# Performance work log

Hardware: AMD Instinct MI355X
Metric: run time of the kernel (lower is better)

## Reference

```python
import jax, jax.numpy as jnp
import numpy as np

N = 262144          # pixels (512x512 image)
F = 2               # in_features (x, y)
K = 13              # num_frequencies
H = 256             # dim_hidden
OUT = 3             # out_features (RGB)
TILES = [1, 4, 16, 64, 256]   # prod(tile_dims[i]) per layer
PE_DIM = F + 2 * F * K        # 54


def setup_inputs() -> dict:
    key = jax.random.key(0)
    ks = jax.random.split(key, 2 * len(TILES) + 3)
    inp = {"coords": jax.random.uniform(ks[0], (N, F), dtype=jnp.float32)}
    d_in = PE_DIM
    for i, t in enumerate(TILES):
        # kaiming-uniform-like scale; biases init to zero as in the module
        bound = float(np.sqrt(6.0 / d_in))
        inp[f"w{i}"] = jax.random.uniform(ks[1 + i], (t, d_in, H), dtype=jnp.float32,
                                           minval=-bound, maxval=bound)
        inp[f"b{i}"] = jnp.zeros((H,), dtype=jnp.float32)
        d_in = H
    bound = float(np.sqrt(6.0 / H))
    inp["w_last"] = jax.random.uniform(ks[-1], (OUT, H), dtype=jnp.float32,
                                        minval=-bound, maxval=bound)
    inp["b_last"] = jnp.zeros((OUT,), dtype=jnp.float32)
    return inp


def _pos_enc(coords):
    # NeRF positional encoding, concat order: coords, then for each freq i,
    # for each feature j: sin(2^i * pi * c_j), cos(2^i * pi * c_j)
    freqs = (2.0 ** jnp.arange(K, dtype=jnp.float32)) * np.pi      # [K]
    ang = coords[:, None, :] * freqs[None, :, None]                # [N, K, F]
    enc = jnp.stack([jnp.sin(ang), jnp.cos(ang)], axis=-1)         # [N, K, F, 2]
    enc = enc.reshape(coords.shape[0], 2 * K * F)
    return jnp.concatenate([coords, enc], axis=-1)                 # [N, PE_DIM]


def reference(coords, w0, b0, w1, b1, w2, b2, w3, b3, w4, b4, w_last, b_last):
    x = _pos_enc(coords)                                           # [N, 54]
    for w, b in ((w0, b0), (w1, b1), (w2, b2), (w3, b3), (w4, b4)):
        t = w.shape[0]
        x = x.reshape(t, -1, x.shape[-1])                          # [T, N/T, d_in]
        x = jnp.einsum('tnd,tdo->tno', x, w) + b                   # per-tile GEMM
        x = jnp.where(x > 0, x, 0.2 * x)                           # LeakyReLU(0.2)
    x = x.reshape(-1, H)                                           # [N, H]
    return x @ w_last.T + b_last                                   # [N, OUT]
```

## Files before the change

kernel.cpp:

```cpp
#include <hip/hip_runtime.h>
#include <stdint.h>

typedef uint32_t u32;
typedef short s16x8 __attribute__((ext_vector_type(8)));
typedef float f32x16 __attribute__((ext_vector_type(16)));
typedef u32 u32x2 __attribute__((ext_vector_type(2)));
typedef u32 u32x4 __attribute__((ext_vector_type(4)));

#define NPIX   262144
#define HD     256

#define FTHR      256
#define PXB       128
#define NBLK      (NPIX / PXB)
#define ACT_LDS   65536

#define B0_OFF  0u
#define B1_OFF  32768u
#define B2_OFF  557056u
#define B3_OFF  2654208u
#define B4_OFF  11042816u
#define BH_OFF  44597248u
#define BLOB_TOTAL 44613632u
#define F_W1 2048u
#define F_W2 34816u
#define F_W3 165888u
#define F_W4 690176u
#define F_WH 2787328u
#define F_END 2788352u

#define ACT_BYTES  131072
#define WBUF_BYTES 16384
#define FB_LDS     (ACT_BYTES + 2 * WBUF_BYTES)

__device__ __forceinline__ u32 bfpair(float a, float b) {
    u32 ua = __builtin_bit_cast(u32, a);
    u32 ub = __builtin_bit_cast(u32, b);
    ua = (ua + 0x7FFFu + ((ua >> 16) & 1u)) >> 16;
    ub = (ub + 0x7FFFu + ((ub >> 16) & 1u)) >> 16;
    return ua | (ub << 16);
}
__device__ __forceinline__ u32 act_off(int row, int colByte) {
    return (u32)((row << 9) + (colByte ^ ((row & 31) << 4)));
}
__device__ __forceinline__ u32 w_off32(int col, int kByte) {
    return (u32)((col << 6) + (kByte ^ (((col >> 1) & 3) << 4)));
}

extern "C" __global__ __launch_bounds__(256)
void loe_prepass(const float* __restrict__ w0, const float* __restrict__ w1,
                 const float* __restrict__ w2, const float* __restrict__ w3,
                 const float* __restrict__ w4, const float* __restrict__ wl,
                 char* __restrict__ ws)
{
    const u32 f = blockIdx.x * 256 + threadIdx.x;
    if (f >= F_END) return;
    float v[8];
    char* dst;
    if (f < F_W1) {
        const u32 kk = f >> 9, fb = (f >> 6) & 7, lane = f & 63;
        const u32 l31 = lane & 31, lhi = lane >> 5;
        const u32 k0 = kk * 16 + lhi * 8, col = fb * 32 + l31;
        #pragma unroll
        for (int j = 0; j < 8; ++j)
            v[j] = (k0 + j < 54) ? w0[(k0 + j) * HD + col] : 0.0f;
        dst = ws + B0_OFF + (size_t)f * 16;
    } else if (f < F_WH) {
        const float* W; size_t boff; u32 fl;
        if (f < F_W2)      { W = w1; boff = B1_OFF; fl = f - F_W1; }
        else if (f < F_W3) { W = w2; boff = B2_OFF; fl = f - F_W2; }
        else if (f < F_W4) { W = w3; boff = B3_OFF; fl = f - F_W3; }
        else               { W = w4; boff = B4_OFF; fl = f - F_W4; }
        const u32 t = fl >> 13, c = fl & 8191;
        const u32 kk = c >> 9, fb = (c >> 6) & 7, lane = c & 63;
        const u32 l31 = lane & 31, lhi = lane >> 5;
        const u32 k0 = kk * 16 + lhi * 8, col = fb * 32 + l31;
        const float* src = W + (size_t)t * 65536 + (size_t)k0 * HD + col;
        #pragma unroll
        for (int j = 0; j < 8; ++j) v[j] = src[(size_t)j * HD];
        dst = ws + boff + (size_t)fl * 16;
    } else {
        const u32 fl = f - F_WH;
        const u32 kk = fl >> 6, lane = fl & 63;
        const u32 l31 = lane & 31, lhi = lane >> 5;
        const u32 k0 = kk * 16 + lhi * 8;
        #pragma unroll
        for (int j = 0; j < 8; ++j)
            v[j] = (l31 < 3) ? wl[l31 * HD + k0 + j] : 0.0f;
        dst = ws + BH_OFF + (size_t)fl * 16;
    }
    u32x4 pk;
    pk.x = bfpair(v[0], v[1]); pk.y = bfpair(v[2], v[3]);
    pk.z = bfpair(v[4], v[5]); pk.w = bfpair(v[6], v[7]);
    *reinterpret_cast<u32x4*>(dst) = pk;
}

extern "C" __global__ __launch_bounds__(FTHR, 2)
void loe_fused_pre(const float* __restrict__ coords,
                   const float* __restrict__ b0, const float* __restrict__ b1,
                   const float* __restrict__ b2, const float* __restrict__ b3,
                   const float* __restrict__ b4, const float* __restrict__ bl,
                   const char* __restrict__ blob,
                   float* __restrict__ out)
{
    extern __shared__ char lds[];

    const int tid  = threadIdx.x;
    const int lane = tid & 63;
    const int wv   = tid >> 6;
    const int l31  = lane & 31;
    const int lhi  = lane >> 5;

    const int bid  = (int)blockIdx.x;
    const int pb   = ((bid & 7) << 8) | (bid >> 3);
    const int pix0 = pb << 7;

    {
        const int p = tid >> 1;
        const int h = tid & 1;
        const float2 c2 = reinterpret_cast<const float2*>(coords)[pix0 + p];
        const float cf[2] = {c2.x, c2.y};
        #pragma unroll
        for (int u = 0; u < 32; u += 2) {
            float v[2];
            #pragma unroll
            for (int q = 0; q < 2; ++q) {
                const int c = h * 32 + u + q;
                float val;
                if (c < 2) val = cf[c];
                else if (c - 2 >= 52) val = 0.0f;
                else {
                    const int e = c - 2;
                    const float a = cf[(e >> 1) & 1] * (float)(1 << (e >> 2));
                    val = (e & 1) ? cospif(a) : sinpif(a);
                }
                v[q] = val;
            }
            *reinterpret_cast<u32*>(lds + act_off(p, (h * 32 + u) * 2)) = bfpair(v[0], v[1]);
        }
    }

    f32x16 acc[4][2];
    const u32 swz = (u32)(l31 << 4);
    u32 abase[4];
    #pragma unroll
    for (int pt = 0; pt < 4; ++pt) abase[pt] = (u32)((pt * 32 + l31) << 9);

    auto init_acc = [&](const float* Bias) {
        #pragma unroll
        for (int ct = 0; ct < 2; ++ct)
            #pragma unroll
            for (int q = 0; q < 4; ++q) {
                const float4 bv = *reinterpret_cast<const float4*>(Bias + wv * 64 + ct * 32 + q * 8 + lhi * 4);
                #pragma unroll
                for (int pt = 0; pt < 4; ++pt) {
                    acc[pt][ct][q * 4 + 0] = bv.x; acc[pt][ct][q * 4 + 1] = bv.y;
                    acc[pt][ct][q * 4 + 2] = bv.z; acc[pt][ct][q * 4 + 3] = bv.w;
                }
            }
    };

    auto epilogue = [&]() {
        #pragma unroll
        for (int ct = 0; ct < 2; ++ct)
            #pragma unroll
            for (int q = 0; q < 4; ++q) {
                const int oc0 = wv * 64 + ct * 32 + q * 8 + lhi * 4;
                #pragma unroll
                for (int pt = 0; pt < 4; ++pt) {
                    float x[4];
                    #pragma unroll
                    for (int j = 0; j < 4; ++j) {
                        const float v = acc[pt][ct][q * 4 + j];
                        x[j] = fmaxf(v, 0.2f * v);
                    }
                    u32x2 wo;
                    wo.x = bfpair(x[0], x[1]);
                    wo.y = bfpair(x[2], x[3]);
                    *reinterpret_cast<u32x2*>(lds + act_off(pt * 32 + l31, oc0 * 2)) = wo;
                }
            }
    };

    auto run_layer = [&](int KK, const char* wbase, const float* Bias) {
        init_acc(Bias);
        __syncthreads();
        const char* f0 = wbase + (size_t)(wv * 2) * 1024 + (size_t)lane * 16;
        u32x4 wA = *reinterpret_cast<const u32x4*>(f0);
        u32x4 wB = *reinterpret_cast<const u32x4*>(f0 + 1024);
        #pragma unroll 4
        for (int kk = 0; kk < KK; ++kk) {
            const int nk = (kk + 1 < KK) ? kk + 1 : kk;
            const u32x4 nA = *reinterpret_cast<const u32x4*>(f0 + (size_t)nk * 8192);
            const u32x4 nB = *reinterpret_cast<const u32x4*>(f0 + (size_t)nk * 8192 + 1024);
            const u32 cb = (u32)(kk * 32 + lhi * 16) ^ swz;
            s16x8 af[4];
            #pragma unroll
            for (int pt = 0; pt < 4; ++pt)
                af[pt] = *reinterpret_cast<const s16x8*>(lds + abase[pt] + cb);
            const s16x8 a = __builtin_bit_cast(s16x8, wA);
            const s16x8 b = __builtin_bit_cast(s16x8, wB);
            #pragma unroll
            for (int pt = 0; pt < 4; ++pt)
                acc[pt][0] = __builtin_amdgcn_mfma_f32_32x32x16_bf16(a, af[pt], acc[pt][0], 0, 0, 0);
            #pragma unroll
            for (int pt = 0; pt < 4; ++pt)
                acc[pt][1] = __builtin_amdgcn_mfma_f32_32x32x16_bf16(b, af[pt], acc[pt][1], 0, 0, 0);
            wA = nA; wB = nB;
        }
        __syncthreads();
        epilogue();
    };

    const char* b0p = blob + B0_OFF;
    const char* b1p = blob + B1_OFF + (size_t)(pb >> 9) * 131072;
    const char* b2p = blob + B2_OFF + (size_t)(pb >> 7) * 131072;
    const char* b3p = blob + B3_OFF + (size_t)(pb >> 5) * 131072;
    const char* b4p = blob + B4_OFF + (size_t)(pb >> 3) * 131072;
    const char* bHp = blob + BH_OFF;

    run_layer(4,  b0p, b0);
    run_layer(16, b1p, b1);
    run_layer(16, b2p, b2);
    run_layer(16, b3p, b3);
    run_layer(16, b4p, b4);

    __syncthreads();
    {
        f32x16 a;
        #pragma unroll
        for (int r = 0; r < 16; ++r) a[r] = 0.0f;
        const u32 hrow = (u32)((wv * 32 + l31) << 9);
        #pragma unroll 4
        for (int kk = 0; kk < 16; ++kk) {
            const u32x4 wh = *reinterpret_cast<const u32x4*>(bHp + (size_t)kk * 1024 + (size_t)lane * 16);
            const u32 cb = (u32)(kk * 32 + lhi * 16) ^ swz;
            const s16x8 af = *reinterpret_cast<const s16x8*>(lds + hrow + cb);
            a = __builtin_amdgcn_mfma_f32_32x32x16_bf16(__builtin_bit_cast(s16x8, wh), af, a, 0, 0, 0);
        }
        if (lhi == 0) {
            const int p = pix0 + wv * 32 + l31;
            out[p * 3 + 0] = a[0] + bl[0];
            out[p * 3 + 1] = a[1] + bl[1];
            out[p * 3 + 2] = a[2] + bl[2];
        }
    }
}

extern "C" __global__ __launch_bounds__(512, 2)
void loe_fused_fb(const float* __restrict__ coords,
                  const float* __restrict__ w0, const float* __restrict__ b0,
                  const float* __restrict__ w1, const float* __restrict__ b1,
                  const float* __restrict__ w2, const float* __restrict__ b2,
                  const float* __restrict__ w3, const float* __restrict__ b3,
                  const float* __restrict__ w4, const float* __restrict__ b4,
                  const float* __restrict__ wl, const float* __restrict__ bl,
                  float* __restrict__ out)
{
    extern __shared__ char lds[];
    const int tid  = threadIdx.x;
    const int lane = tid & 63;
    const int wv   = tid >> 6;
    const int wr   = wv >> 2;
    const int wc   = wv & 3;
    const int l31  = lane & 31;
    const int lhi  = lane >> 5;
    const int bid  = (int)blockIdx.x;
    const int pb   = ((bid & 7) << 7) | (bid >> 3);
    const int pix0 = pb << 8;
    const int scol = tid & 255;
    const int kh   = tid >> 8;

    float st[16];
    auto load_plain = [&](const float* W, int s) {
        const float* src = W + (size_t)(s * 32 + kh * 16) * HD + scol;
        #pragma unroll
        for (int j = 0; j < 16; ++j) st[j] = src[(size_t)j * HD];
    };
    auto load_guard = [&](const float* W, int s) {
        #pragma unroll
        for (int j = 0; j < 16; ++j) {
            const int k = s * 32 + kh * 16 + j;
            st[j] = (k < 54) ? W[k * HD + scol] : 0.0f;
        }
    };
    load_guard(w0, 0);
    {
        const int p = tid >> 1;
        const int h = tid & 1;
        const float2 c2 = reinterpret_cast<const float2*>(coords)[pix0 + p];
        const float cf[2] = {c2.x, c2.y};
        #pragma unroll
        for (int u = 0; u < 32; u += 2) {
            float v[2];
            #pragma unroll
            for (int q = 0; q < 2; ++q) {
                const int c = h * 32 + u + q;
                float val;
                if (c < 2) val = cf[c];
                else if (c - 2 >= 52) val = 0.0f;
                else {
                    const int e = c - 2;
                    const float a = cf[(e >> 1) & 1] * (float)(1 << (e >> 2));
                    val = (e & 1) ? cospif(a) : sinpif(a);
                }
                v[q] = val;
            }
            *reinterpret_cast<u32*>(lds + act_off(p, (h * 32 + u) * 2)) = bfpair(v[0], v[1]);
        }
    }
    f32x16 acc[4][2];
    int g = 0;
    auto epilogue = [&](const float* Bias) {
        #pragma unroll
        for (int ct = 0; ct < 2; ++ct)
            #pragma unroll
            for (int q = 0; q < 4; ++q) {
                const int oc0 = wc * 64 + ct * 32 + q * 8 + lhi * 4;
                const float4 bv = *reinterpret_cast<const float4*>(Bias + oc0);
                const float bj[4] = {bv.x, bv.y, bv.z, bv.w};
                #pragma unroll
                for (int pt = 0; pt < 4; ++pt) {
                    const int p = wr * 128 + pt * 32 + l31;
                    float x[4];
                    #pragma unroll
                    for (int j = 0; j < 4; ++j) {
                        float v = acc[pt][ct][q * 4 + j] + bj[j];
                        x[j] = (v > 0.0f) ? v : 0.2f * v;
                    }
                    u32x2 wv2;
                    wv2.x = bfpair(x[0], x[1]);
                    wv2.y = bfpair(x[2], x[3]);
                    *reinterpret_cast<u32x2*>(lds + act_off(p, oc0 * 2)) = wv2;
                }
            }
    };
    auto run_layer = [&](int S, const float* Wcur, const float* Wnext,
                         const float* Bias, bool guard) {
        #pragma unroll
        for (int pt = 0; pt < 4; ++pt)
            #pragma unroll
            for (int ct = 0; ct < 2; ++ct)
                #pragma unroll
                for (int r = 0; r < 16; ++r) acc[pt][ct][r] = 0.0f;
        for (int s = 0; s < S; ++s) {
            char* wbw = lds + ACT_BYTES + ((g & 1) ? WBUF_BYTES : 0);
            u32x4 pk0, pk1;
            pk0.x = bfpair(st[0], st[1]);   pk0.y = bfpair(st[2], st[3]);
            pk0.z = bfpair(st[4], st[5]);   pk0.w = bfpair(st[6], st[7]);
            pk1.x = bfpair(st[8], st[9]);   pk1.y = bfpair(st[10], st[11]);
            pk1.z = bfpair(st[12], st[13]); pk1.w = bfpair(st[14], st[15]);
            *reinterpret_cast<u32x4*>(wbw + w_off32(scol, kh * 32))      = pk0;
            *reinterpret_cast<u32x4*>(wbw + w_off32(scol, kh * 32 + 16)) = pk1;
            if (s + 1 < S) { if (guard) load_guard(Wcur, s + 1); else load_plain(Wcur, s + 1); }
            else if (Wnext) load_plain(Wnext, 0);
            __syncthreads();
            #pragma unroll
            for (int kt = 0; kt < 2; ++kt) {
                const int kb = kt * 32 + lhi * 16;
                s16x8 wf[2], af[4];
                #pragma unroll
                for (int ct = 0; ct < 2; ++ct)
                    wf[ct] = *reinterpret_cast<const s16x8*>(wbw + w_off32(wc * 64 + ct * 32 + l31, kb));
                #pragma unroll
                for (int pt = 0; pt < 4; ++pt)
                    af[pt] = *reinterpret_cast<const s16x8*>(lds + act_off(wr * 128 + pt * 32 + l31, s * 64 + kb));
                #pragma unroll
                for (int pt = 0; pt < 4; ++pt)
                    #pragma unroll
                    for (int ct = 0; ct < 2; ++ct)
                        acc[pt][ct] = __builtin_amdgcn_mfma_f32_32x32x16_bf16(wf[ct], af[pt], acc[pt][ct], 0, 0, 0);
            }
            ++g;
            __syncthreads();
        }
        epilogue(Bias);
        __syncthreads();
    };
    const float* w1t = w1 + (size_t)(pb >> 8) * 65536;
    const float* w2t = w2 + (size_t)(pb >> 6) * 65536;
    const float* w3t = w3 + (size_t)(pb >> 4) * 65536;
    const float* w4t = w4 + (size_t)(pb >> 2) * 65536;
    __syncthreads();
    run_layer(2, w0,  w1t, b0, true);
    run_layer(8, w1t, w2t, b1, false);
    run_layer(8, w2t, w3t, b2, false);
    run_layer(8, w3t, w4t, b3, false);
    run_layer(8, w4t, nullptr, b4, false);
    char* hw = lds + ACT_BYTES;
    #pragma unroll
    for (int rep = 0; rep < 2; ++rep) {
        const int task = rep * 512 + tid;
        const int col  = task & 31;
        const int kg   = task >> 5;
        float v[8];
        #pragma unroll
        for (int j = 0; j < 8; ++j)
            v[j] = (col < 3) ? wl[col * HD + kg * 8 + j] : 0.0f;
        u32x4 pk;
        pk.x = bfpair(v[0], v[1]); pk.y = bfpair(v[2], v[3]);
        pk.z = bfpair(v[4], v[5]); pk.w = bfpair(v[6], v[7]);
        *reinterpret_cast<u32x4*>(hw + col * 512 + ((kg * 16) ^ ((col & 7) << 4))) = pk;
    }
    __syncthreads();
    {
        f32x16 a;
        #pragma unroll
        for (int r = 0; r < 16; ++r) a[r] = 0.0f;
        #pragma unroll
        for (int kt = 0; kt < 16; ++kt) {
            const int kb = kt * 32 + lhi * 16;
            s16x8 wf = *reinterpret_cast<const s16x8*>(hw + l31 * 512 + (kb ^ ((l31 & 7) << 4)));
            s16x8 af = *reinterpret_cast<const s16x8*>(lds + act_off(wv * 32 + l31, kb));
            a = __builtin_amdgcn_mfma_f32_32x32x16_bf16(wf, af, a, 0, 0, 0);
        }
        if (lhi == 0) {
            const int p = pix0 + wv * 32 + l31;
            out[p * 3 + 0] = a[0] + bl[0];
            out[p * 3 + 1] = a[1] + bl[1];
            out[p * 3 + 2] = a[2] + bl[2];
        }
    }
}

extern "C" void kernel_launch(void* const* d_in, const int* in_sizes, int n_in,
                              void* d_out, int out_size, void* d_ws, size_t ws_size,
                              hipStream_t stream) {
    (void)in_sizes; (void)n_in; (void)out_size;
    const float* coords = (const float*)d_in[0];
    const float* w0 = (const float*)d_in[1];  const float* b0 = (const float*)d_in[2];
    const float* w1 = (const float*)d_in[3];  const float* b1 = (const float*)d_in[4];
    const float* w2 = (const float*)d_in[5];  const float* b2 = (const float*)d_in[6];
    const float* w3 = (const float*)d_in[7];  const float* b3 = (const float*)d_in[8];
    const float* w4 = (const float*)d_in[9];  const float* b4 = (const float*)d_in[10];
    const float* wl = (const float*)d_in[11]; const float* bl = (const float*)d_in[12];
    float* out = (float*)d_out;

    if (ws_size >= (size_t)BLOB_TOTAL) {
        (void)hipFuncSetAttribute((const void*)loe_fused_pre,
                                  hipFuncAttributeMaxDynamicSharedMemorySize, ACT_LDS);
        loe_prepass<<<dim3((F_END + 255) / 256), dim3(256), 0, stream>>>(
            w0, w1, w2, w3, w4, wl, (char*)d_ws);
        loe_fused_pre<<<dim3(NBLK), dim3(FTHR), ACT_LDS, stream>>>(
            coords, b0, b1, b2, b3, b4, bl, (const char*)d_ws, out);
    } else {
        (void)hipFuncSetAttribute((const void*)loe_fused_fb,
                                  hipFuncAttributeMaxDynamicSharedMemorySize, FB_LDS);
        loe_fused_fb<<<dim3(NPIX / 256), dim3(512), FB_LDS, stream>>>(
            coords, w0, b0, w1, b1, w2, b2, w3, b3, w4, b4, wl, bl, out);
    }
}
```

Before: 185.8 us.

## Double threads per block so each wave computes 32 output channels

Raises the block from 4 to 8 waves, giving each wave a 32-channel slice of the 256 outputs instead of 64. That halves the accumulator registers per wave (4 instead of 8 f32x16 tiles). The K loop is unrolled by two with separate weight prefetches, and the final head runs only on the first four waves. The aim is more resident waves to hide latency. In exchange, every wave now reads the full activation tile from LDS, doubling LDS read traffic per MFMA.

```diff
diff --git a/kernel.cpp b/kernel.cpp
--- a/kernel.cpp
+++ b/kernel.cpp
@@ -10,7 +10,7 @@
 #define NPIX   262144
 #define HD     256
 
-#define FTHR      256
+#define FTHR      512
 #define PXB       128
 #define NBLK      (NPIX / PXB)
 #define ACT_LDS   65536
@@ -95,7 +95,7 @@
     *reinterpret_cast<u32x4*>(dst) = pk;
 }
 
-extern "C" __global__ __launch_bounds__(FTHR, 2)
+extern "C" __global__ __launch_bounds__(FTHR, 4)
 void loe_fused_pre(const float* __restrict__ coords,
                    const float* __restrict__ b0, const float* __restrict__ b1,
                    const float* __restrict__ b2, const float* __restrict__ b3,
@@ -116,16 +116,16 @@
     const int pix0 = pb << 7;
 
     {
-        const int p = tid >> 1;
-        const int h = tid & 1;
+        const int p = tid >> 2;
+        const int h = tid & 3;
         const float2 c2 = reinterpret_cast<const float2*>(coords)[pix0 + p];
         const float cf[2] = {c2.x, c2.y};
         #pragma unroll
-        for (int u = 0; u < 32; u += 2) {
+        for (int u = 0; u < 16; u += 2) {
             float v[2];
             #pragma unroll
             for (int q = 0; q < 2; ++q) {
-                const int c = h * 32 + u + q;
+                const int c = h * 16 + u + q;
                 float val;
                 if (c < 2) val = cf[c];
                 else if (c - 2 >= 52) val = 0.0f;
@@ -136,11 +136,11 @@
                 }
                 v[q] = val;
             }
-            *reinterpret_cast<u32*>(lds + act_off(p, (h * 32 + u) * 2)) = bfpair(v[0], v[1]);
-        }
-    }
-
-    f32x16 acc[4][2];
+            *reinterpret_cast<u32*>(lds + act_off(p, (h * 16 + u) * 2)) = bfpair(v[0], v[1]);
+        }
+    }
+
+    f32x16 acc[4];
     const u32 swz = (u32)(l31 << 4);
     u32 abase[4];
     #pragma unroll
@@ -148,64 +148,70 @@
 
     auto init_acc = [&](const float* Bias) {
         #pragma unroll
-        for (int ct = 0; ct < 2; ++ct)
-            #pragma unroll
-            for (int q = 0; q < 4; ++q) {
-                const float4 bv = *reinterpret_cast<const float4*>(Bias + wv * 64 + ct * 32 + q * 8 + lhi * 4);
-                #pragma unroll
-                for (int pt = 0; pt < 4; ++pt) {
-                    acc[pt][ct][q * 4 + 0] = bv.x; acc[pt][ct][q * 4 + 1] = bv.y;
-                    acc[pt][ct][q * 4 + 2] = bv.z; acc[pt][ct][q * 4 + 3] = bv.w;
+        for (int q = 0; q < 4; ++q) {
+            const float4 bv = *reinterpret_cast<const float4*>(Bias + wv * 32 + q * 8 + lhi * 4);
+            #pragma unroll
+            for (int pt = 0; pt < 4; ++pt) {
+                acc[pt][q * 4 + 0] = bv.x; acc[pt][q * 4 + 1] = bv.y;
+                acc[pt][q * 4 + 2] = bv.z; acc[pt][q * 4 + 3] = bv.w;
+            }
+        }
+    };
+
+    auto epilogue = [&]() {
+        #pragma unroll
+        for (int q = 0; q < 4; ++q) {
+            const int oc0 = wv * 32 + q * 8 + lhi * 4;
+            #pragma unroll
+            for (int pt = 0; pt < 4; ++pt) {
+                float x[4];
+                #pragma unroll
+                for (int j = 0; j < 4; ++j) {
+                    const float v = acc[pt][q * 4 + j];
+                    x[j] = fmaxf(v, 0.2f * v);
                 }
-            }
-    };
-
-    auto epilogue = [&]() {
-        #pragma unroll
-        for (int ct = 0; ct < 2; ++ct)
-            #pragma unroll
-            for (int q = 0; q < 4; ++q) {
-                const int oc0 = wv * 64 + ct * 32 + q * 8 + lhi * 4;
-                #pragma unroll
-                for (int pt = 0; pt < 4; ++pt) {
-                    float x[4];
-                    #pragma unroll
-                    for (int j = 0; j < 4; ++j) {
-                        const float v = acc[pt][ct][q * 4 + j];
-                        x[j] = fmaxf(v, 0.2f * v);
-                    }
-                    u32x2 wo;
-                    wo.x = bfpair(x[0], x[1]);
-                    wo.y = bfpair(x[2], x[3]);
-                    *reinterpret_cast<u32x2*>(lds + act_off(pt * 32 + l31, oc0 * 2)) = wo;
-                }
-            }
+                u32x2 wo;
+                wo.x = bfpair(x[0], x[1]);
+                wo.y = bfpair(x[2], x[3]);
+                *reinterpret_cast<u32x2*>(lds + act_off(pt * 32 + l31, oc0 * 2)) = wo;
+            }
+        }
     };
 
     auto run_layer = [&](int KK, const char* wbase, const float* Bias) {
         init_acc(Bias);
         __syncthreads();
-        const char* f0 = wbase + (size_t)(wv * 2) * 1024 + (size_t)lane * 16;
+        const char* f0 = wbase + (size_t)wv * 1024 + (size_t)lane * 16;
         u32x4 wA = *reinterpret_cast<const u32x4*>(f0);
-        u32x4 wB = *reinterpret_cast<const u32x4*>(f0 + 1024);
+        u32x4 wB = *reinterpret_cast<const u32x4*>(f0 + 8192);
         #pragma unroll 4
-        for (int kk = 0; kk < KK; ++kk) {
-            const int nk = (kk + 1 < KK) ? kk + 1 : kk;
-            const u32x4 nA = *reinterpret_cast<const u32x4*>(f0 + (size_t)nk * 8192);
-            const u32x4 nB = *reinterpret_cast<const u32x4*>(f0 + (size_t)nk * 8192 + 1024);
-            const u32 cb = (u32)(kk * 32 + lhi * 16) ^ swz;
-            s16x8 af[4];
-            #pragma unroll
-            for (int pt = 0; pt < 4; ++pt)
-                af[pt] = *reinterpret_cast<const s16x8*>(lds + abase[pt] + cb);
-            const s16x8 a = __builtin_bit_cast(s16x8, wA);
-            const s16x8 b = __builtin_bit_cast(s16x8, wB);
-            #pragma unroll
-            for (int pt = 0; pt < 4; ++pt)
-                acc[pt][0] = __builtin_amdgcn_mfma_f32_32x32x16_bf16(a, af[pt], acc[pt][0], 0, 0, 0);
-            #pragma unroll
-            for (int pt = 0; pt < 4; ++pt)
-                acc[pt][1] = __builtin_amdgcn_mfma_f32_32x32x16_bf16(b, af[pt], acc[pt][1], 0, 0, 0);
+        for (int kk = 0; kk < KK; kk += 2) {
+            const int n2 = (kk + 2 < KK) ? kk + 2 : kk;
+            const int n3 = (kk + 3 < KK) ? kk + 3 : KK - 1;
+            const u32x4 nA = *reinterpret_cast<const u32x4*>(f0 + (size_t)n2 * 8192);
+            const u32x4 nB = *reinterpret_cast<const u32x4*>(f0 + (size_t)n3 * 8192);
+            {
+                const u32 cb = (u32)(kk * 32 + lhi * 16) ^ swz;
+                s16x8 af[4];
+                #pragma unroll
+                for (int pt = 0; pt < 4; ++pt)
+                    af[pt] = *reinterpret_cast<const s16x8*>(lds + abase[pt] + cb);
+                const s16x8 a = __builtin_bit_cast(s16x8, wA);
+                #pragma unroll
+                for (int pt = 0; pt < 4; ++pt)
+                    acc[pt] = __builtin_amdgcn_mfma_f32_32x32x16_bf16(a, af[pt], acc[pt], 0, 0, 0);
+            }
+            {
+                const u32 cb = (u32)((kk + 1) * 32 + lhi * 16) ^ swz;
+                s16x8 af[4];
+                #pragma unroll
+                for (int pt = 0; pt < 4; ++pt)
+                    af[pt] = *reinterpret_cast<const s16x8*>(lds + abase[pt] + cb);
+                const s16x8 a = __builtin_bit_cast(s16x8, wB);
+                #pragma unroll
+                for (int pt = 0; pt < 4; ++pt)
+                    acc[pt] = __builtin_amdgcn_mfma_f32_32x32x16_bf16(a, af[pt], acc[pt], 0, 0, 0);
+            }
             wA = nA; wB = nB;
         }
         __syncthreads();
@@ -226,7 +232,7 @@
     run_layer(16, b4p, b4);
 
     __syncthreads();
-    {
+    if (wv < 4) {
         f32x16 a;
         #pragma unroll
         for (int r = 0; r < 16; ++r) a[r] = 0.0f;
```

Result: slower. 191.8 us (+3.2%).
